# Kernel optimization log

Measured on AMD Instinct MI355X. Metric: run time of the kernel, lower is better.

Reference implementation:

```python
import jax, jax.numpy as jnp
import numpy as np

N_NODES = 100000
N_EDGES = 3200000
IN_DIM = 128
OUT_DIM = 128


def setup_inputs() -> dict:
    key = jax.random.key(0)
    k1, k2, k3, k4, k5 = jax.random.split(key, 5)
    features = jax.random.normal(k1, (N_NODES, IN_DIM), dtype=jnp.float32)
    edge_src = jax.random.randint(k2, (N_EDGES,), 0, N_NODES, dtype=jnp.int32)
    edge_dst = jax.random.randint(k3, (N_EDGES,), 0, N_NODES, dtype=jnp.int32)
    edge_vals = jax.random.uniform(k4, (N_EDGES,), dtype=jnp.float32)
    # kaiming_normal_ on [in, out] with fan_in = in
    weight = jax.random.normal(k5, (IN_DIM, OUT_DIM), dtype=jnp.float32) * np.sqrt(2.0 / IN_DIM)
    bias = jnp.zeros((OUT_DIM,), dtype=jnp.float32)
    return {
        "features": features,
        "edge_src": edge_src,
        "edge_dst": edge_dst,
        "edge_vals": edge_vals,
        "weight": weight,
        "bias": bias,
    }


def reference(features, edge_src, edge_dst, edge_vals, weight, bias):
    # h = X @ W  : [N, out]
    h = features @ weight
    # SpMM: out[dst] += A[dst, src] * h[src]   (COO edge-list aggregation)
    msgs = h[edge_src] * edge_vals[:, None]          # [E, out]
    agg = jax.ops.segment_sum(msgs, edge_dst, num_segments=N_NODES)
    return agg + bias
```

## Files before the change

kernel.cpp:

```cpp
#include <hip/hip_runtime.h>

#define IN_DIM 128
#define OUT_DIM 128
#define BIN_SHIFT 7
#define BIN_NODES 128
#define NBIN_MAX 800
#define CAP1 4736
#define TILE_A 3072

typedef __attribute__((ext_vector_type(8))) short bf16x8;
typedef __attribute__((ext_vector_type(4))) float f32x4;
typedef __attribute__((ext_vector_type(2))) float f32x2;

__device__ inline unsigned short f2bf(float f) {
    unsigned u = __float_as_uint(f);
    unsigned r = (u + 0x7fff + ((u >> 16) & 1)) >> 16;
    return (unsigned short)r;
}
__device__ inline float bflo(unsigned h) { return __uint_as_float(h << 16); }
__device__ inline float bfhi(unsigned h) { return __uint_as_float(h & 0xffff0000u); }

__global__ __launch_bounds__(256) void pack_w_zero(const float* __restrict__ W,
                                                   unsigned short* __restrict__ Wpack,
                                                   int* __restrict__ gcur, int nbin) {
    int idx = blockIdx.x * 256 + threadIdx.x;
    if (idx < nbin) gcur[idx] = 0;
    if (idx >= 16384) return;
    int j = idx & 7;
    int lane = (idx >> 3) & 63;
    int kc = (idx >> 9) & 3;
    int tn = idx >> 11;
    int k = kc * 32 + (lane >> 4) * 8 + j;
    int n = tn * 16 + (lane & 15);
    Wpack[idx] = f2bf(W[k * OUT_DIM + n]);
}

struct BinSmem {
    int2 eL[TILE_A];
    int hist[NBIN_MAX];
    int dbase[NBIN_MAX];
    unsigned short bL[TILE_A];
};

__global__ __launch_bounds__(256) void phase1(
    const int* __restrict__ src, const int* __restrict__ dst,
    const float* __restrict__ vals, int* __restrict__ gcur,
    int2* __restrict__ entries, int n_edges, int nbin, int nA,
    const float* __restrict__ X, const unsigned short* __restrict__ Wpack,
    unsigned short* __restrict__ Hb, int n_rows, int nG) {
    __shared__ BinSmem sm;

    int b = blockIdx.x;
    int isGemm, widx;
    if (b < 2 * nG) {
        isGemm = (b & 1) == 0;
        widx = b >> 1;
    } else {
        isGemm = 0;
        widx = nG + (b - 2 * nG);
    }

    const int tid = threadIdx.x;

    if (!isGemm) {
        const int base = widx * TILE_A;
        const int n0 = n_edges - base;
        if (n0 <= 0) return;
        const int n = (n0 < TILE_A) ? n0 : TILE_A;

        for (int i = tid; i < nbin; i += 256) sm.hist[i] = 0;
        __syncthreads();

        for (int i = tid; i < n; i += 256) {
            int d = dst[base + i];
            int s = src[base + i];
            float v = vals[base + i];
            int bin = d >> BIN_SHIFT;
            sm.eL[i] = make_int2(s | ((d & (BIN_NODES - 1)) << 17), __float_as_int(v));
            sm.bL[i] = (unsigned short)bin;
            atomicAdd(&sm.hist[bin], 1);
        }
        __syncthreads();

        for (int l = tid; l < nbin; l += 256) {
            int c = sm.hist[l];
            sm.dbase[l] = (c > 0) ? atomicAdd(&gcur[l], c) : 0;
            sm.hist[l] = 0;
        }
        __syncthreads();

        for (int i = tid; i < n; i += 256) {
            int bin = sm.bL[i];
            int pos = sm.dbase[bin] + atomicAdd(&sm.hist[bin], 1);
            if (pos < CAP1) entries[(long long)bin * CAP1 + pos] = sm.eL[i];
        }
        return;
    }

    int strip = widx * 4 + (tid >> 6);
    long long m0 = (long long)strip * 32;
    if (m0 >= n_rows) return;
    int lane = tid & 63;
    int quad = lane >> 4;
    int low = lane & 15;

    const bf16x8* B = (const bf16x8*)Wpack;

    long long r0 = m0 + low;
    long long r1 = m0 + 16 + low;
    if (r1 >= n_rows) r1 = n_rows - 1;
    if (r0 >= n_rows) r0 = n_rows - 1;

    f32x4 acc[2][8] = {};

#pragma unroll
    for (int kc = 0; kc < 4; ++kc) {
        const float4* p0 = (const float4*)(X + r0 * IN_DIM + kc * 32 + quad * 8);
        const float4* p1 = (const float4*)(X + r1 * IN_DIM + kc * 32 + quad * 8);
        float4 x0a = p0[0], x0b = p0[1];
        float4 x1a = p1[0], x1b = p1[1];
        bf16x8 afr0, afr1;
        afr0[0] = f2bf(x0a.x); afr0[1] = f2bf(x0a.y); afr0[2] = f2bf(x0a.z); afr0[3] = f2bf(x0a.w);
        afr0[4] = f2bf(x0b.x); afr0[5] = f2bf(x0b.y); afr0[6] = f2bf(x0b.z); afr0[7] = f2bf(x0b.w);
        afr1[0] = f2bf(x1a.x); afr1[1] = f2bf(x1a.y); afr1[2] = f2bf(x1a.z); afr1[3] = f2bf(x1a.w);
        afr1[4] = f2bf(x1b.x); afr1[5] = f2bf(x1b.y); afr1[6] = f2bf(x1b.z); afr1[7] = f2bf(x1b.w);
#pragma unroll
        for (int tn = 0; tn < 8; ++tn) {
            bf16x8 bfr = B[(tn * 4 + kc) * 64 + lane];
            acc[0][tn] = __builtin_amdgcn_mfma_f32_16x16x32_bf16(afr0, bfr, acc[0][tn], 0, 0, 0);
            acc[1][tn] = __builtin_amdgcn_mfma_f32_16x16x32_bf16(afr1, bfr, acc[1][tn], 0, 0, 0);
        }
    }

#pragma unroll
    for (int t = 0; t < 2; ++t) {
#pragma unroll
        for (int tn = 0; tn < 8; ++tn) {
#pragma unroll
            for (int r = 0; r < 4; ++r) {
                long long row = m0 + t * 16 + quad * 4 + r;
                if (row < n_rows) {
                    int col = tn * 16 + low;
                    Hb[row * OUT_DIM + col] = f2bf(acc[t][tn][r]);
                }
            }
        }
    }
}

__global__ __launch_bounds__(512) void binB_gather(
    const int2* __restrict__ entries, const int* __restrict__ gcur,
    const unsigned short* __restrict__ Hb, const float* __restrict__ bias,
    float* __restrict__ out, int n_nodes) {
    __shared__ int2 ent[CAP1];
    __shared__ int hist[BIN_NODES];
    __shared__ int dbase[BIN_NODES];
    __shared__ int cur[BIN_NODES];

    const int bin = blockIdx.x;
    const int tid = threadIdx.x;
    const int cnt = min(gcur[bin], CAP1);
    const long long base = (long long)bin * CAP1;

    if (tid < BIN_NODES) hist[tid] = 0;
    __syncthreads();

    int2 e[10];
    bool ok[10];
#pragma unroll
    for (int j = 0; j < 10; ++j) {
        int i = tid + j * 512;
        ok[j] = (i < cnt);
        if (ok[j]) e[j] = entries[base + i];
    }
#pragma unroll
    for (int j = 0; j < 10; ++j)
        if (ok[j]) atomicAdd(&hist[(e[j].x >> 17) & (BIN_NODES - 1)], 1);
    __syncthreads();

    if (tid < BIN_NODES) dbase[tid] = hist[tid];
    __syncthreads();
    for (int d = 1; d < BIN_NODES; d <<= 1) {
        int v = 0;
        if (tid < BIN_NODES && tid >= d) v = dbase[tid - d];
        __syncthreads();
        if (tid < BIN_NODES) dbase[tid] += v;
        __syncthreads();
    }
    if (tid < BIN_NODES) {
        int ex = dbase[tid] - hist[tid];
        dbase[tid] = ex;
        cur[tid] = ex;
    }
    __syncthreads();

#pragma unroll
    for (int j = 0; j < 10; ++j)
        if (ok[j]) {
            int l = (e[j].x >> 17) & (BIN_NODES - 1);
            int pos = atomicAdd(&cur[l], 1);
            ent[pos] = e[j];
        }
    __syncthreads();

    const int wave = tid >> 6;
    const int lane = tid & 63;
    const int node0 = bin * BIN_NODES;
    float2 bb = ((const float2*)bias)[lane];

    for (int ln = wave * 16; ln < wave * 16 + 16; ++ln) {
        int node = node0 + ln;
        if (node >= n_nodes) break;
        int beg = dbase[ln];
        int end = beg + hist[ln];

        f32x2 acc;
        acc[0] = bb.x; acc[1] = bb.y;

        int i = beg;
        for (; i + 8 <= end; i += 8) {
            int2 c[8];
#pragma unroll
            for (int j = 0; j < 8; ++j) c[j] = ent[i + j];
            unsigned h[8];
#pragma unroll
            for (int j = 0; j < 8; ++j)
                h[j] = *(const unsigned*)(Hb + (long long)(c[j].x & 0x1ffff) * OUT_DIM + lane * 2);
#pragma unroll
            for (int j = 0; j < 8; ++j) {
                float v = __int_as_float(c[j].y);
                f32x2 hv; hv[0] = bflo(h[j]); hv[1] = bfhi(h[j]);
                f32x2 vv; vv[0] = v; vv[1] = v;
                acc += vv * hv;
            }
        }
        for (; i < end; ++i) {
            int2 c0 = ent[i];
            unsigned h0 = *(const unsigned*)(Hb + (long long)(c0.x & 0x1ffff) * OUT_DIM + lane * 2);
            float v = __int_as_float(c0.y);
            f32x2 hv; hv[0] = bflo(h0); hv[1] = bfhi(h0);
            f32x2 vv; vv[0] = v; vv[1] = v;
            acc += vv * hv;
        }

        float2 res; res.x = acc[0]; res.y = acc[1];
        ((float2*)(out + (long long)node * OUT_DIM))[lane] = res;
    }
}

extern "C" void kernel_launch(void* const* d_in, const int* in_sizes, int n_in,
                              void* d_out, int out_size, void* d_ws, size_t ws_size,
                              hipStream_t stream) {
    const float* features  = (const float*)d_in[0];
    const int* edge_src    = (const int*)d_in[1];
    const int* edge_dst    = (const int*)d_in[2];
    const float* edge_vals = (const float*)d_in[3];
    const float* weight    = (const float*)d_in[4];
    const float* bias      = (const float*)d_in[5];

    const int n_nodes = in_sizes[0] / IN_DIM;
    const int n_edges = in_sizes[1];
    const int nbin = (n_nodes + BIN_NODES - 1) / BIN_NODES;

    int2* entries       = (int2*)d_ws;
    unsigned short* Hb  = (unsigned short*)(entries + (long long)nbin * CAP1);
    unsigned short* Wp  = Hb + (long long)n_nodes * OUT_DIM;
    int* gcur           = (int*)(Wp + 16384);

    float* out = (float*)d_out;

    pack_w_zero<<<64, 256, 0, stream>>>(weight, Wp, gcur, nbin);

    const int nA = (n_edges + TILE_A - 1) / TILE_A;
    const int n_strips = (n_nodes + 31) / 32;
    const int nG = (n_strips + 3) / 4;
    phase1<<<nA + nG, 256, 0, stream>>>(edge_src, edge_dst, edge_vals, gcur,
                                        entries, n_edges, nbin, nA,
                                        features, Wp, Hb, n_nodes, nG);

    binB_gather<<<nbin, 512, 0, stream>>>(entries, gcur, Hb, bias, out, n_nodes);
}
```

Baseline: 304.9 us.

## Partition bin counters into eight sub-buckets and deepen gather unroll to sixteen

Phase1 now spreads each bin's global atomic counter and entry storage across eight partitions chosen by tile index. This is meant to cut contention on the per-bin global atomics. The gather kernel reads all partitions into LDS and reassembles them, and its inner gather loop is unrolled to 16 loads to keep more memory requests in flight. The risks are that more global counters must be read, that per-partition capacity overflows on skewed bins, and that register pressure rises from the 16-entry staging arrays.

After: 300.6 us. About the same (-1.4%).

```diff
diff --git a/kernel.cpp b/kernel.cpp
--- a/kernel.cpp
+++ b/kernel.cpp
@@ -5,7 +5,9 @@
 #define BIN_SHIFT 7
 #define BIN_NODES 128
 #define NBIN_MAX 800
-#define CAP1 4736
+#define NPART 8
+#define CAPX 1024
+#define CAP_LDS 4864
 #define TILE_A 3072
 
 typedef __attribute__((ext_vector_type(8))) short bf16x8;
@@ -22,9 +24,9 @@
 
 __global__ __launch_bounds__(256) void pack_w_zero(const float* __restrict__ W,
                                                    unsigned short* __restrict__ Wpack,
-                                                   int* __restrict__ gcur, int nbin) {
+                                                   int* __restrict__ gcur, int nbin8) {
     int idx = blockIdx.x * 256 + threadIdx.x;
-    if (idx < nbin) gcur[idx] = 0;
+    if (idx < nbin8) gcur[idx] = 0;
     if (idx >= 16384) return;
     int j = idx & 7;
     int lane = (idx >> 3) & 63;
@@ -63,6 +65,7 @@
     const int tid = threadIdx.x;
 
     if (!isGemm) {
+        const int part = widx & (NPART - 1);
         const int base = widx * TILE_A;
         const int n0 = n_edges - base;
         if (n0 <= 0) return;
@@ -84,7 +87,7 @@
 
         for (int l = tid; l < nbin; l += 256) {
             int c = sm.hist[l];
-            sm.dbase[l] = (c > 0) ? atomicAdd(&gcur[l], c) : 0;
+            sm.dbase[l] = (c > 0) ? atomicAdd(&gcur[part * nbin + l], c) : 0;
             sm.hist[l] = 0;
         }
         __syncthreads();
@@ -92,7 +95,8 @@
         for (int i = tid; i < n; i += 256) {
             int bin = sm.bL[i];
             int pos = sm.dbase[bin] + atomicAdd(&sm.hist[bin], 1);
-            if (pos < CAP1) entries[(long long)bin * CAP1 + pos] = sm.eL[i];
+            if (pos < CAPX)
+                entries[((long long)(part * nbin + bin)) * CAPX + pos] = sm.eL[i];
         }
         return;
     }
@@ -151,31 +155,43 @@
 __global__ __launch_bounds__(512) void binB_gather(
     const int2* __restrict__ entries, const int* __restrict__ gcur,
     const unsigned short* __restrict__ Hb, const float* __restrict__ bias,
-    float* __restrict__ out, int n_nodes) {
-    __shared__ int2 ent[CAP1];
+    float* __restrict__ out, int n_nodes, int nbin) {
+    __shared__ int2 ent[CAP_LDS];
     __shared__ int hist[BIN_NODES];
     __shared__ int dbase[BIN_NODES];
     __shared__ int cur[BIN_NODES];
 
     const int bin = blockIdx.x;
     const int tid = threadIdx.x;
-    const int cnt = min(gcur[bin], CAP1);
-    const long long base = (long long)bin * CAP1;
+
+    int scnt[NPART], sbase[NPART];
+    int tot = 0;
+#pragma unroll
+    for (int s = 0; s < NPART; ++s) {
+        int c = gcur[s * nbin + bin];
+        scnt[s] = (c < CAPX) ? c : CAPX;
+        sbase[s] = tot;
+        tot += scnt[s];
+    }
 
     if (tid < BIN_NODES) hist[tid] = 0;
     __syncthreads();
 
-    int2 e[10];
-    bool ok[10];
-#pragma unroll
-    for (int j = 0; j < 10; ++j) {
-        int i = tid + j * 512;
-        ok[j] = (i < cnt);
-        if (ok[j]) e[j] = entries[base + i];
-    }
-#pragma unroll
-    for (int j = 0; j < 10; ++j)
-        if (ok[j]) atomicAdd(&hist[(e[j].x >> 17) & (BIN_NODES - 1)], 1);
+    int2 e[2 * NPART];
+    bool ok[2 * NPART];
+#pragma unroll
+    for (int s = 0; s < NPART; ++s) {
+#pragma unroll
+        for (int k = 0; k < 2; ++k) {
+            int i = tid + k * 512;
+            int idx = s * 2 + k;
+            ok[idx] = (i < scnt[s]) && (sbase[s] + i < CAP_LDS);
+            if (ok[idx]) e[idx] = entries[((long long)(s * nbin + bin)) * CAPX + i];
+        }
+    }
+#pragma unroll
+    for (int idx = 0; idx < 2 * NPART; ++idx)
+        if (ok[idx]) atomicAdd(&hist[(e[idx].x >> 17) & (BIN_NODES - 1)], 1);
     __syncthreads();
 
     if (tid < BIN_NODES) dbase[tid] = hist[tid];
@@ -195,11 +211,11 @@
     __syncthreads();
 
 #pragma unroll
-    for (int j = 0; j < 10; ++j)
-        if (ok[j]) {
-            int l = (e[j].x >> 17) & (BIN_NODES - 1);
+    for (int idx = 0; idx < 2 * NPART; ++idx)
+        if (ok[idx]) {
+            int l = (e[idx].x >> 17) & (BIN_NODES - 1);
             int pos = atomicAdd(&cur[l], 1);
-            ent[pos] = e[j];
+            ent[pos] = e[idx];
         }
     __syncthreads();
 
@@ -207,6 +223,7 @@
     const int lane = tid & 63;
     const int node0 = bin * BIN_NODES;
     float2 bb = ((const float2*)bias)[lane];
+    const unsigned short* hrow = Hb + lane * 2;
 
     for (int ln = wave * 16; ln < wave * 16 + 16; ++ln) {
         int node = node0 + ln;
@@ -218,25 +235,41 @@
         acc[0] = bb.x; acc[1] = bb.y;
 
         int i = beg;
+        for (; i + 16 <= end; i += 16) {
+            unsigned h[16];
+            float v[16];
+#pragma unroll
+            for (int j = 0; j < 16; ++j) {
+                int2 c = ent[i + j];
+                v[j] = __int_as_float(c.y);
+                h[j] = *(const unsigned*)(hrow + (long long)(c.x & 0x1ffff) * OUT_DIM);
+            }
+#pragma unroll
+            for (int j = 0; j < 16; ++j) {
+                f32x2 hv; hv[0] = bflo(h[j]); hv[1] = bfhi(h[j]);
+                f32x2 vv; vv[0] = v[j]; vv[1] = v[j];
+                acc += vv * hv;
+            }
+        }
         for (; i + 8 <= end; i += 8) {
-            int2 c[8];
-#pragma unroll
-            for (int j = 0; j < 8; ++j) c[j] = ent[i + j];
             unsigned h[8];
-#pragma unroll
-            for (int j = 0; j < 8; ++j)
-                h[j] = *(const unsigned*)(Hb + (long long)(c[j].x & 0x1ffff) * OUT_DIM + lane * 2);
+            float v[8];
 #pragma unroll
             for (int j = 0; j < 8; ++j) {
-                float v = __int_as_float(c[j].y);
+                int2 c = ent[i + j];
+                v[j] = __int_as_float(c.y);
+                h[j] = *(const unsigned*)(hrow + (long long)(c.x & 0x1ffff) * OUT_DIM);
+            }
+#pragma unroll
+            for (int j = 0; j < 8; ++j) {
                 f32x2 hv; hv[0] = bflo(h[j]); hv[1] = bfhi(h[j]);
-                f32x2 vv; vv[0] = v; vv[1] = v;
+                f32x2 vv; vv[0] = v[j]; vv[1] = v[j];
                 acc += vv * hv;
             }
         }
         for (; i < end; ++i) {
             int2 c0 = ent[i];
-            unsigned h0 = *(const unsigned*)(Hb + (long long)(c0.x & 0x1ffff) * OUT_DIM + lane * 2);
+            unsigned h0 = *(const unsigned*)(hrow + (long long)(c0.x & 0x1ffff) * OUT_DIM);
             float v = __int_as_float(c0.y);
             f32x2 hv; hv[0] = bflo(h0); hv[1] = bfhi(h0);
             f32x2 vv; vv[0] = v; vv[1] = v;
@@ -263,13 +296,13 @@
     const int nbin = (n_nodes + BIN_NODES - 1) / BIN_NODES;
 
     int2* entries       = (int2*)d_ws;
-    unsigned short* Hb  = (unsigned short*)(entries + (long long)nbin * CAP1);
+    unsigned short* Hb  = (unsigned short*)(entries + (long long)NPART * nbin * CAPX);
     unsigned short* Wp  = Hb + (long long)n_nodes * OUT_DIM;
     int* gcur           = (int*)(Wp + 16384);
 
     float* out = (float*)d_out;
 
-    pack_w_zero<<<64, 256, 0, stream>>>(weight, Wp, gcur, nbin);
+    pack_w_zero<<<64, 256, 0, stream>>>(weight, Wp, gcur, NPART * nbin);
 
     const int nA = (n_edges + TILE_A - 1) / TILE_A;
     const int n_strips = (n_nodes + 31) / 32;
@@ -278,5 +311,5 @@
                                         entries, n_edges, nbin, nA,
                                         features, Wp, Hb, n_nodes, nG);
 
-    binB_gather<<<nbin, 512, 0, stream>>>(entries, gcur, Hb, bias, out, n_nodes);
-}
+    binB_gather<<<nbin, 512, 0, stream>>>(entries, gcur, Hb, bias, out, n_nodes, nbin);
+}
```
